# Kernel tuning notes

Hardware: AMD Instinct MI355X
Metric: run time of the kernel (lower is better)

The kernel has to match this reference:

```python
import jax, jax.numpy as jnp
import numpy as np


def _conv1d(x, w, b, pad):
    # x: (BN, Cin, L), w: (Cout, Cin, K) torch OIH layout
    y = jax.lax.conv_general_dilated(x, w, window_strides=(1,), padding=[(pad, pad)],
                                     dimension_numbers=('NCH', 'OIH', 'NCH'))
    return y + b[None, :, None]


def _mask_conv(m, k):
    # all-ones kernel conv then >=1 threshold (matches constant-init mask convs, no_grad)
    w = jnp.ones((1, 1, k), m.dtype)
    y = jax.lax.conv_general_dilated(m, w, window_strides=(1,), padding=[((k - 1) // 2, (k - 1) // 2)],
                                     dimension_numbers=('NCH', 'OIH', 'NCH'))
    return (y >= 1.0).astype(m.dtype)


def _branch(x, m, w1, b1, w2, b2, k):
    pad = (k - 1) // 2
    o = jax.nn.relu(_conv1d(x, w1, b1, pad))
    m = jax.lax.stop_gradient(_mask_conv(m, k))
    o = o * m
    o = jax.nn.relu(_conv1d(o, w2, b2, pad))
    m = jax.lax.stop_gradient(_mask_conv(m, k))
    return o * m


def _forward(all_xanes, all_xanes_mask, all_elem_info, all_elem_mask,
             w_b1c1, b_b1c1, w_b1c2, b_b1c2,
             w_b2c1, b_b2c1, w_b2c2, b_b2c2,
             w_b3c1, b_b3c1, w_b3c2, b_b3c2,
             w_xfc, b_xfc,
             w_float, b_float, atom_emb, type_emb,
             w_fuse, b_fuse,
             in_w, in_b, out_w, out_b,
             w_fc1, b_fc1, w_fc2, b_fc2):
    B, N, L = all_xanes.shape
    E, H = 64, 4
    dh = E // H
    # ---- MultiScaleXANESExtractor ----
    x = all_xanes.reshape(B * N, 1, L)
    m3 = jnp.broadcast_to(all_xanes_mask.reshape(B * N, 1, 1).astype(jnp.float32), (B * N, 1, L))
    o1 = _branch(x, m3, w_b1c1, b_b1c1, w_b1c2, b_b1c2, 3)
    o2 = _branch(x, m3, w_b2c1, b_b2c1, w_b2c2, b_b2c2, 5)
    o3 = _branch(x, m3, w_b3c1, b_b3c1, w_b3c2, b_b3c2, 7)
    cat = jnp.concatenate([o1, o2, o3], axis=1)  # (BN, 384, L)
    pooled = cat.reshape(B * N, 384, 10, L // 10).mean(-1).reshape(B * N, -1)  # AdaptiveAvgPool1d(10)
    xfeat = (pooled @ w_xfc.T + b_xfc).reshape(B, N, -1)  # (B, N, 32)
    valid = (m3.sum(axis=(1, 2)) > 0).astype(jnp.float32).reshape(B, N, 1)
    xfeat = xfeat * valid
    # ---- ElementsFeatureProcessor (vectorized gathers) ----
    maskf = all_elem_mask.astype(jnp.float32)
    masked = all_elem_info * maskf[..., None]
    ff = jax.nn.relu(masked[..., :5] @ w_float.T + b_float)  # (B, N, 16)
    an = masked[..., 5].astype(jnp.int32)
    et = masked[..., 6].astype(jnp.int32)
    valid_e = (maskf >= 0.5)
    inrange = (an >= 1) & (an <= 94)
    take = (valid_e & inrange).astype(jnp.float32)[..., None]
    ez = atom_emb[jnp.clip(an, 0, 94)] * take            # (B, N, 8)
    ety = type_emb[jnp.clip(et, 0, 5)] * take            # (B, N, 4)
    ff = ff * valid_e.astype(jnp.float32)[..., None]
    efeat = jnp.concatenate([ff, ez, ety], axis=-1) * maskf[..., None]  # (B, N, 28)
    # ---- FuseElementAndXANES ----
    fused = jnp.concatenate([xfeat, efeat], axis=-1) @ w_fuse.T + b_fuse
    fused = fused * maskf[..., None]  # (B, N, 64)
    # ---- AttentionAggregator (nn.MultiheadAttention, batch_first) ----
    qkv = fused @ in_w.T + in_b
    q, k, v = jnp.split(qkv, 3, axis=-1)
    q = q.reshape(B, N, H, dh)
    k = k.reshape(B, N, H, dh)
    v = v.reshape(B, N, H, dh)
    scores = jnp.einsum('bqhd,bkhd->bhqk', q, k) / jnp.sqrt(jnp.float32(dh))
    keymask = (maskf >= 0.5)
    scores = jnp.where(keymask[:, None, None, :], scores, jnp.float32(-1e30))
    attn = jax.nn.softmax(scores, axis=-1)
    ao = jnp.einsum('bhqk,bkhd->bqhd', attn, v).reshape(B, N, E)
    ao = ao @ out_w.T + out_b
    ao = ao * maskf[..., None]
    pooled2 = ao.sum(axis=1) / (maskf.sum(axis=1, keepdims=True) + 1e-8)
    h = jax.nn.relu(pooled2 @ w_fc1.T + b_fc1)
    return h @ w_fc2.T + b_fc2  # (B, num_classes)


def setup_inputs():
    key = jax.random.key(0)
    ks = jax.random.split(key, 40)
    B, N, L = 32, 16, 200
    all_xanes = jax.random.normal(ks[0], (B, N, L), jnp.float32)
    all_xanes_mask = jax.random.randint(ks[1], (B, N), 0, 2).astype(jnp.float32)
    ef = jax.random.normal(ks[2], (B, N, 7), jnp.float32)
    an = jax.random.randint(ks[3], (B, N), 1, 95).astype(jnp.float32)
    et = jax.random.randint(ks[4], (B, N), 0, 6).astype(jnp.float32)
    all_elem_info = ef.at[..., 5].set(an).at[..., 6].set(et)
    all_elem_mask = jax.random.randint(ks[5], (B, N), 0, 2).astype(jnp.float32)
    all_elem_mask = all_elem_mask.at[:, 0].set(1.0)  # avoid fully-padded rows (NaN softmax)

    def p(k, shape):
        return jax.random.normal(k, shape, jnp.float32) * 0.05

    inp = dict(all_xanes=all_xanes, all_xanes_mask=all_xanes_mask,
               all_elem_info=all_elem_info, all_elem_mask=all_elem_mask,
               w_b1c1=p(ks[6], (64, 1, 3)), b_b1c1=p(ks[7], (64,)),
               w_b1c2=p(ks[8], (128, 64, 3)), b_b1c2=p(ks[9], (128,)),
               w_b2c1=p(ks[10], (64, 1, 5)), b_b2c1=p(ks[11], (64,)),
               w_b2c2=p(ks[12], (128, 64, 5)), b_b2c2=p(ks[13], (128,)),
               w_b3c1=p(ks[14], (64, 1, 7)), b_b3c1=p(ks[15], (64,)),
               w_b3c2=p(ks[16], (128, 64, 7)), b_b3c2=p(ks[17], (128,)),
               w_xfc=p(ks[18], (32, 3840)), b_xfc=p(ks[19], (32,)),
               w_float=p(ks[20], (16, 5)), b_float=p(ks[21], (16,)),
               atom_emb=p(ks[22], (95, 8)), type_emb=p(ks[23], (6, 4)),
               w_fuse=p(ks[24], (64, 60)), b_fuse=p(ks[25], (64,)),
               in_w=p(ks[26], (192, 64)), in_b=p(ks[27], (192,)),
               out_w=p(ks[28], (64, 64)), out_b=p(ks[29], (64,)),
               w_fc1=p(ks[30], (64, 64)), b_fc1=p(ks[31], (64,)),
               w_fc2=p(ks[32], (1, 64)), b_fc2=p(ks[33], (1,)))
    return inp


def reference(all_xanes, all_xanes_mask, all_elem_info, all_elem_mask,
              w_b1c1, b_b1c1, w_b1c2, b_b1c2,
              w_b2c1, b_b2c1, w_b2c2, b_b2c2,
              w_b3c1, b_b3c1, w_b3c2, b_b3c2,
              w_xfc, b_xfc, w_float, b_float, atom_emb, type_emb,
              w_fuse, b_fuse, in_w, in_b, out_w, out_b,
              w_fc1, b_fc1, w_fc2, b_fc2):
    return _forward(all_xanes, all_xanes_mask, all_elem_info, all_elem_mask,
                    w_b1c1, b_b1c1, w_b1c2, b_b1c2,
                    w_b2c1, b_b2c1, w_b2c2, b_b2c2,
                    w_b3c1, b_b3c1, w_b3c2, b_b3c2,
                    w_xfc, b_xfc, w_float, b_float, atom_emb, type_emb,
                    w_fuse, b_fuse, in_w, in_b, out_w, out_b,
                    w_fc1, b_fc1, w_fc2, b_fc2)
```

## Files before the change

### kernel.cpp

```cpp
#include <hip/hip_runtime.h>
#include <math.h>

typedef float f32x4 __attribute__((ext_vector_type(4)));
typedef short short8 __attribute__((ext_vector_type(8)));

__device__ __forceinline__ short bf16r(float f) {
    union { float f; unsigned u; } x; x.f = f;
    unsigned u = x.u + 0x7fffu + ((x.u >> 16) & 1u);
    return (short)(u >> 16);
}

template<int K>
__device__ __forceinline__ void pack_branch(const float* __restrict__ w2,
                                            short* __restrict__ wpack, int u) {
    int lane = u & 63;
    int kb   = (u >> 6) & 1;
    int rem  = u >> 7;
    int j = rem % K, c = rem / K;
    int co  = c * 16 + (lane & 15);
    int cib = kb * 32 + 8 * ((lane >> 4) & 3);
    short8 v;
    #pragma unroll
    for (int i = 0; i < 8; ++i)
        v[i] = bf16r(w2[(co * 64 + (cib + i)) * K + j]);
    *reinterpret_cast<short8*>(wpack + (size_t)u * 8) = v;
}

__global__ __launch_bounds__(256) void pack_kernel(
    const float* __restrict__ w23, const float* __restrict__ w25,
    const float* __restrict__ w27,
    short* __restrict__ wp3, short* __restrict__ wp5, short* __restrict__ wp7)
{
    int tid = blockIdx.x * 256 + threadIdx.x;
    const int n3 = 8 * 3 * 2 * 64;
    const int n5 = 8 * 5 * 2 * 64;
    const int n7 = 8 * 7 * 2 * 64;
    if (tid < n3)                pack_branch<3>(w23, wp3, tid);
    else if (tid < n3 + n5)      pack_branch<5>(w25, wp5, tid - n3);
    else if (tid < n3 + n5 + n7) pack_branch<7>(w27, wp7, tid - n3 - n5);
}

template<int K, int LT0, int NLT>
__device__ __forceinline__ void mfma_pass2(
    const short* __restrict__ t1s,
    const short8* __restrict__ wpB0, const short8* __restrict__ wpB1,
    int lane, f32x4* accA, f32x4* accB)
{
    constexpr int PAD = (K - 1) / 2;
    const int lane15 = lane & 15;
    const int g8 = 8 * ((lane >> 4) & 3);
    short8 bA = wpB0[0], bB = wpB1[0];
    #pragma unroll 1
    for (int m = 0; m < 2 * K - 1; ++m) {
        const short8 nA = wpB0[(m + 1) * 64];
        const short8 nB = wpB1[(m + 1) * 64];
        const int j = m >> 1, kb = m & 1;
        const int r = LT0 * 16 + lane15 + 3 + j - PAD;
        const int col = (kb * 32 + g8) ^ ((r & 7) << 3);
        const short* ab = &t1s[r * 64 + col];
        #pragma unroll
        for (int lt = 0; lt < NLT; ++lt) {
            const short8 af = *reinterpret_cast<const short8*>(ab + lt * 1024);
            accA[lt] = __builtin_amdgcn_mfma_f32_16x16x32_bf16(af, bA, accA[lt], 0, 0, 0);
            accB[lt] = __builtin_amdgcn_mfma_f32_16x16x32_bf16(af, bB, accB[lt], 0, 0, 0);
        }
        bA = nA; bB = nB;
    }
    {
        const int m = 2 * K - 1;
        const int j = m >> 1, kb = m & 1;
        const int r = LT0 * 16 + lane15 + 3 + j - PAD;
        const int col = (kb * 32 + g8) ^ ((r & 7) << 3);
        const short* ab = &t1s[r * 64 + col];
        #pragma unroll
        for (int lt = 0; lt < NLT; ++lt) {
            const short8 af = *reinterpret_cast<const short8*>(ab + lt * 1024);
            accA[lt] = __builtin_amdgcn_mfma_f32_16x16x32_bf16(af, bA, accA[lt], 0, 0, 0);
            accB[lt] = __builtin_amdgcn_mfma_f32_16x16x32_bf16(af, bB, accB[lt], 0, 0, 0);
        }
    }
}

template<int GV, int LT0, int NLT>
__device__ __forceinline__ void pool_accum(const f32x4* acc, float bb, float* pb) {
    #pragma unroll
    for (int lt = 0; lt < NLT; ++lt) {
        #pragma unroll
        for (int r4 = 0; r4 < 4; ++r4) {
            const int l = (LT0 + lt) * 16 + 4 * GV + r4;
            if (l < 200)
                pb[l / 20] += fmaxf(acc[lt][r4] + bb, 0.0f);
        }
    }
}

template<int K, int LT0, int NLT>
__device__ __forceinline__ void do_pass2(
    const short* __restrict__ t1s,
    const short8* __restrict__ wpB0, const short8* __restrict__ wpB1,
    int lane, float bb0, float bb1, float* pb0, float* pb1)
{
    const int g = (lane >> 4) & 3;
    f32x4 accA[NLT], accB[NLT];
    #pragma unroll
    for (int i = 0; i < NLT; ++i) {
        f32x4 z = {0.f, 0.f, 0.f, 0.f};
        accA[i] = z; accB[i] = z;
    }
    mfma_pass2<K, LT0, NLT>(t1s, wpB0, wpB1, lane, accA, accB);
    if      (g == 0) { pool_accum<0, LT0, NLT>(accA, bb0, pb0); pool_accum<0, LT0, NLT>(accB, bb1, pb1); }
    else if (g == 1) { pool_accum<1, LT0, NLT>(accA, bb0, pb0); pool_accum<1, LT0, NLT>(accB, bb1, pb1); }
    else if (g == 2) { pool_accum<2, LT0, NLT>(accA, bb0, pb0); pool_accum<2, LT0, NLT>(accB, bb1, pb1); }
    else             { pool_accum<3, LT0, NLT>(accA, bb0, pb0); pool_accum<3, LT0, NLT>(accB, bb1, pb1); }
}

template<int K>
__device__ __forceinline__ void branch_body(
    const int bn, const int t,
    const float* __restrict__ x,
    const float* __restrict__ w1, const float* __restrict__ b1,
    const float* __restrict__ b2, const short* __restrict__ wpack,
    const float* __restrict__ w_xfc_br, float* __restrict__ xfeatP_br,
    float* xs, short* t1s, float* pooled_s, float* b2s)
{
    constexpr int PAD = (K - 1) / 2;
    const int lane = t & 63;
    const int w    = t >> 6;
    const int lane15 = lane & 15;

    if (t < 208) xs[t] = 0.0f;
    for (int idx = t; idx < 32 * 64; idx += 256) {
        int rr = idx >> 6;
        int row = (rr < 3) ? rr : (200 + rr);
        t1s[row * 64 + (idx & 63)] = 0;
    }
    if (t < 128) b2s[t] = b2[t];
    __syncthreads();

    if (t < 200) xs[3 + t] = x[bn * 200 + t];
    __syncthreads();

    {
        float w1_0 = w1[lane * K + 0], w1_1 = w1[lane * K + 1], w1_2 = w1[lane * K + 2];
        float w1_3 = 0.f, w1_4 = 0.f, w1_5 = 0.f, w1_6 = 0.f;
        if (K > 3) { w1_3 = w1[lane * K + 3]; w1_4 = w1[lane * K + 4]; }
        if (K > 5) { w1_5 = w1[lane * K + 5]; w1_6 = w1[lane * K + 6]; }
        const float b1r = b1[lane];
        #pragma unroll 1
        for (int ch = 0; ch < 2; ++ch) {
            const int lb = 50 * w + 25 * ch;
            float xr[31];
            #pragma unroll
            for (int i = 0; i < 31; ++i) xr[i] = xs[lb + i];
            #pragma unroll
            for (int ll = 0; ll < 25; ++ll) {
                float a = b1r;
                a = fmaf(w1_0, xr[ll + 3 - PAD + 0], a);
                a = fmaf(w1_1, xr[ll + 3 - PAD + 1], a);
                a = fmaf(w1_2, xr[ll + 3 - PAD + 2], a);
                if (K > 3) {
                    a = fmaf(w1_3, xr[ll + 3 - PAD + 3], a);
                    a = fmaf(w1_4, xr[ll + 3 - PAD + 4], a);
                }
                if (K > 5) {
                    a = fmaf(w1_5, xr[ll + 3 - PAD + 5], a);
                    a = fmaf(w1_6, xr[ll + 3 - PAD + 6], a);
                }
                const int row = lb + ll + 3;
                t1s[row * 64 + (lane ^ ((row & 7) << 3))] = bf16r(fmaxf(a, 0.0f));
            }
        }
    }
    __syncthreads();

    const int c0 = 2 * w, c1 = 2 * w + 1;
    const int coA = c0 * 16 + lane15, coB = c1 * 16 + lane15;
    const float bb0 = b2s[coA], bb1 = b2s[coB];
    const short8* wpB0 = reinterpret_cast<const short8*>(wpack)
                         + (size_t)(c0 * 2 * K) * 64 + lane;
    const short8* wpB1 = reinterpret_cast<const short8*>(wpack)
                         + (size_t)(c1 * 2 * K) * 64 + lane;

    float pb0[10], pb1[10];
    #pragma unroll
    for (int b = 0; b < 10; ++b) { pb0[b] = 0.0f; pb1[b] = 0.0f; }

    do_pass2<K, 0, 7>(t1s, wpB0, wpB1, lane, bb0, bb1, pb0, pb1);
    do_pass2<K, 7, 6>(t1s, wpB0, wpB1, lane, bb0, bb1, pb0, pb1);

    #pragma unroll
    for (int b = 0; b < 10; ++b) {
        pb0[b] += __shfl_xor(pb0[b], 16);
        pb0[b] += __shfl_xor(pb0[b], 32);
        pb1[b] += __shfl_xor(pb1[b], 16);
        pb1[b] += __shfl_xor(pb1[b], 32);
    }
    if (lane < 16) {
        #pragma unroll
        for (int b = 0; b < 10; ++b) {
            pooled_s[coA * 10 + b] = pb0[b];
            pooled_s[coB * 10 + b] = pb1[b];
        }
    }
    __syncthreads();

    {
        const int o = t >> 3, part = t & 7;
        const f32x4* wr4 = reinterpret_cast<const f32x4*>(w_xfc_br + o * 3840);
        const f32x4* pp4 = reinterpret_cast<const f32x4*>(pooled_s);
        float s0 = 0.0f, s1 = 0.0f;
        #pragma unroll
        for (int i = 0; i < 40; ++i) {
            const f32x4 wv = wr4[part + 8 * i];
            const f32x4 pv = pp4[part + 8 * i];
            float s = wv[0] * pv[0];
            s = fmaf(wv[1], pv[1], s);
            s = fmaf(wv[2], pv[2], s);
            s = fmaf(wv[3], pv[3], s);
            if (i & 1) s1 += s; else s0 += s;
        }
        float a = s0 + s1;
        a += __shfl_xor(a, 1);
        a += __shfl_xor(a, 2);
        a += __shfl_xor(a, 4);
        if (part == 0) xfeatP_br[bn * 32 + o] = a * 0.05f;
    }
}

__global__ __launch_bounds__(256, 4) void branch_fused(
    const float* __restrict__ x, const float* __restrict__ xmask,
    const float* __restrict__ w1_3, const float* __restrict__ b1_3,
    const float* __restrict__ b2_3, const short* __restrict__ wp3,
    const float* __restrict__ w1_5, const float* __restrict__ b1_5,
    const float* __restrict__ b2_5, const short* __restrict__ wp5,
    const float* __restrict__ w1_7, const float* __restrict__ b1_7,
    const float* __restrict__ b2_7, const short* __restrict__ wp7,
    const float* __restrict__ w_xfc, float* __restrict__ xfeatP)
{
    __shared__ float xs[208];
    __shared__ short t1s[232 * 64];
    __shared__ __align__(16) float pooled_s[1280];
    __shared__ float b2s[128];

    const int bx = blockIdx.x;
    const int br = bx % 3;
    const int bn = bx / 3;
    const int t  = threadIdx.x;

    if (xmask[bn] == 0.0f) return;

    if (br == 0)
        branch_body<3>(bn, t, x, w1_3, b1_3, b2_3, wp3,
                       w_xfc,        xfeatP,             xs, t1s, pooled_s, b2s);
    else if (br == 1)
        branch_body<5>(bn, t, x, w1_5, b1_5, b2_5, wp5,
                       w_xfc + 1280, xfeatP + 512 * 32,  xs, t1s, pooled_s, b2s);
    else
        branch_body<7>(bn, t, x, w1_7, b1_7, b2_7, wp7,
                       w_xfc + 2560, xfeatP + 1024 * 32, xs, t1s, pooled_s, b2s);
}

__global__ __launch_bounds__(256, 1) void tail_kernel(
    const float* __restrict__ xfeatP,
    const float* __restrict__ b_xfc,
    const float* __restrict__ xmaskp,
    const float* __restrict__ elem_info,
    const float* __restrict__ emaskp,
    const float* __restrict__ w_float, const float* __restrict__ b_float,
    const float* __restrict__ atom_emb, const float* __restrict__ type_emb,
    const float* __restrict__ w_fuse,  const float* __restrict__ b_fuse,
    const float* __restrict__ in_w,    const float* __restrict__ in_b,
    const float* __restrict__ out_w,   const float* __restrict__ out_b,
    const float* __restrict__ w_fc1,   const float* __restrict__ b_fc1,
    const float* __restrict__ w_fc2,   const float* __restrict__ b_fc2,
    float* __restrict__ out)
{
    const int b = blockIdx.x;
    const int t = threadIdx.x;

    __shared__ __align__(16) float fu[16][60];
    __shared__ __align__(16) float fused[16][64];
    __shared__ __align__(16) float qkvs[16][196];
    __shared__ __align__(16) float sc[4][16][16];
    __shared__ __align__(16) float ao[16][64];
    __shared__ __align__(16) float aoo[16][64];
    __shared__ float p2s[64];
    __shared__ float hs[64];
    __shared__ float em[16];

    if (t < 16) em[t] = emaskp[b * 16 + t];

    for (int d = t; d < 512; d += 256) {
        int n = d >> 5, o = d & 31;
        const int bn = b * 16 + n;
        float a = xfeatP[bn * 32 + o]
                + xfeatP[(512 + bn) * 32 + o]
                + xfeatP[(1024 + bn) * 32 + o];
        fu[n][o] = (a + b_xfc[o]) * xmaskp[bn];
    }
    {
        int n = t >> 4, slot = t & 15;
        float m  = emaskp[b * 16 + n];
        float vE = (m >= 0.5f) ? 1.0f : 0.0f;
        const float* ei = elem_info + (b * 16 + n) * 7;
        float a = b_float[slot];
        #pragma unroll
        for (int i = 0; i < 5; ++i)
            a = fmaf(ei[i] * m, w_float[slot * 5 + i], a);
        fu[n][32 + slot] = fmaxf(a, 0.0f) * vE * m;

        int an = (int)(ei[5] * m);
        int et = (int)(ei[6] * m);
        float take = (vE != 0.0f && an >= 1 && an <= 94) ? 1.0f : 0.0f;
        int anc = an < 0 ? 0 : (an > 94 ? 94 : an);
        int etc = et < 0 ? 0 : (et > 5 ? 5 : et);
        if (slot < 8)
            fu[n][48 + slot] = atom_emb[anc * 8 + slot] * take * m;
        else if (slot < 12)
            fu[n][56 + (slot - 8)] = type_emb[etc * 4 + (slot - 8)] * take * m;
    }
    __syncthreads();

    for (int d = t; d < 1024; d += 256) {
        int n = d >> 6, o = d & 63;
        const f32x4* wr4 = reinterpret_cast<const f32x4*>(w_fuse + o * 60);
        const f32x4* fr4 = reinterpret_cast<const f32x4*>(&fu[n][0]);
        float a0 = b_fuse[o], a1 = 0.0f;
        #pragma unroll
        for (int i = 0; i < 15; ++i) {
            const f32x4 wv = wr4[i];
            const f32x4 fv = fr4[i];
            float s = wv[0] * fv[0];
            s = fmaf(wv[1], fv[1], s);
            s = fmaf(wv[2], fv[2], s);
            s = fmaf(wv[3], fv[3], s);
            if (i & 1) a1 += s; else a0 += s;
        }
        fused[n][o] = (a0 + a1) * em[n];
    }
    __syncthreads();

    for (int d = t; d < 3072; d += 256) {
        int n = d / 192, rr = d - n * 192;
        const f32x4* wr4 = reinterpret_cast<const f32x4*>(in_w + rr * 64);
        const f32x4* fr4 = reinterpret_cast<const f32x4*>(&fused[n][0]);
        float a0 = in_b[rr], a1 = 0.0f;
        #pragma unroll
        for (int i = 0; i < 16; ++i) {
            const f32x4 wv = wr4[i];
            const f32x4 fv = fr4[i];
            float s = wv[0] * fv[0];
            s = fmaf(wv[1], fv[1], s);
            s = fmaf(wv[2], fv[2], s);
            s = fmaf(wv[3], fv[3], s);
            if (i & 1) a1 += s; else a0 += s;
        }
        qkvs[n][rr] = a0 + a1;
    }
    __syncthreads();

    for (int d = t; d < 1024; d += 256) {
        int h = d >> 8, i = (d >> 4) & 15, j = d & 15;
        const f32x4* qi = reinterpret_cast<const f32x4*>(&qkvs[i][h * 16]);
        const f32x4* kj = reinterpret_cast<const f32x4*>(&qkvs[j][64 + h * 16]);
        float a = 0.0f;
        #pragma unroll
        for (int q4 = 0; q4 < 4; ++q4) {
            const f32x4 qv = qi[q4];
            const f32x4 kv = kj[q4];
            a = fmaf(qv[0], kv[0], a);
            a = fmaf(qv[1], kv[1], a);
            a = fmaf(qv[2], kv[2], a);
            a = fmaf(qv[3], kv[3], a);
        }
        a *= 0.25f;
        if (em[j] < 0.5f) a = -1e30f;
        sc[h][i][j] = a;
    }
    __syncthreads();

    if (t < 64) {
        int h = t >> 4, i = t & 15;
        float mx = -3.4e38f;
        #pragma unroll
        for (int j = 0; j < 16; ++j) mx = fmaxf(mx, sc[h][i][j]);
        float e[16];
        float s = 0.0f;
        #pragma unroll
        for (int j = 0; j < 16; ++j) { e[j] = expf(sc[h][i][j] - mx); s += e[j]; }
        float inv = 1.0f / s;
        #pragma unroll
        for (int j = 0; j < 16; ++j) sc[h][i][j] = e[j] * inv;
    }
    __syncthreads();

    for (int d = t; d < 1024; d += 256) {
        int n = d >> 6, e = d & 63, h = e >> 4;
        float a = 0.0f;
        #pragma unroll
        for (int j = 0; j < 16; ++j)
            a = fmaf(sc[h][n][j], qkvs[j][128 + e], a);
        ao[n][e] = a;
    }
    __syncthreads();

    for (int d = t; d < 1024; d += 256) {
        int n = d >> 6, o = d & 63;
        const f32x4* wr4 = reinterpret_cast<const f32x4*>(out_w + o * 64);
        const f32x4* ar4 = reinterpret_cast<const f32x4*>(&ao[n][0]);
        float a0 = out_b[o], a1 = 0.0f;
        #pragma unroll
        for (int i = 0; i < 16; ++i) {
            const f32x4 wv = wr4[i];
            const f32x4 av = ar4[i];
            float s = wv[0] * av[0];
            s = fmaf(wv[1], av[1], s);
            s = fmaf(wv[2], av[2], s);
            s = fmaf(wv[3], av[3], s);
            if (i & 1) a1 += s; else a0 += s;
        }
        aoo[n][o] = (a0 + a1) * em[n];
    }
    __syncthreads();

    if (t < 64) {
        float s = 0.0f, ms = 0.0f;
        #pragma unroll
        for (int n = 0; n < 16; ++n) { s += aoo[n][t]; ms += em[n]; }
        p2s[t] = s / (ms + 1e-8f);
    }
    __syncthreads();

    if (t < 64) {
        const f32x4* wr4 = reinterpret_cast<const f32x4*>(w_fc1 + t * 64);
        const f32x4* pr4 = reinterpret_cast<const f32x4*>(p2s);
        float a0 = b_fc1[t], a1 = 0.0f;
        #pragma unroll
        for (int i = 0; i < 16; ++i) {
            const f32x4 wv = wr4[i];
            const f32x4 pv = pr4[i];
            float s = wv[0] * pv[0];
            s = fmaf(wv[1], pv[1], s);
            s = fmaf(wv[2], pv[2], s);
            s = fmaf(wv[3], pv[3], s);
            if (i & 1) a1 += s; else a0 += s;
        }
        hs[t] = fmaxf(a0 + a1, 0.0f);
    }
    __syncthreads();

    if (t < 64) {
        float v = hs[t] * w_fc2[t];
        #pragma unroll
        for (int d2 = 32; d2 >= 1; d2 >>= 1) v += __shfl_xor(v, d2);
        if (t == 0) out[b] = v + b_fc2[0];
    }
}

extern "C" void kernel_launch(void* const* d_in, const int* in_sizes, int n_in,
                              void* d_out, int out_size, void* d_ws, size_t ws_size,
                              hipStream_t stream)
{
    (void)in_sizes; (void)n_in; (void)out_size; (void)ws_size;
    const float* x     = (const float*)d_in[0];
    const float* xmask = (const float*)d_in[1];
    const float* einfo = (const float*)d_in[2];
    const float* emask = (const float*)d_in[3];

    float* xfeatP = (float*)d_ws;
    short* wp3 = (short*)(xfeatP + 3 * 512 * 32);
    short* wp5 = wp3 + 24576;
    short* wp7 = wp5 + 40960;

    pack_kernel<<<60, 256, 0, stream>>>(
        (const float*)d_in[6], (const float*)d_in[10], (const float*)d_in[14],
        wp3, wp5, wp7);

    branch_fused<<<1536, 256, 0, stream>>>(x, xmask,
        (const float*)d_in[4],  (const float*)d_in[5],  (const float*)d_in[7],  wp3,
        (const float*)d_in[8],  (const float*)d_in[9],  (const float*)d_in[11], wp5,
        (const float*)d_in[12], (const float*)d_in[13], (const float*)d_in[15], wp7,
        (const float*)d_in[16], xfeatP);

    tail_kernel<<<32, 256, 0, stream>>>(xfeatP,
        (const float*)d_in[17], xmask, einfo, emask,
        (const float*)d_in[18], (const float*)d_in[19],
        (const float*)d_in[20], (const float*)d_in[21],
        (const float*)d_in[22], (const float*)d_in[23],
        (const float*)d_in[24], (const float*)d_in[25],
        (const float*)d_in[26], (const float*)d_in[27],
        (const float*)d_in[28], (const float*)d_in[29],
        (const float*)d_in[30], (const float*)d_in[31],
        (float*)d_out);
}
```

Before: 70.19 us.

## Fuse branch and tail kernels into one launch with per-batch completion counters

Merges the branch convolution kernel and the tail attention kernel into a single persistent-style launch. The first 32 blocks spin-wait on per-batch atomic counters until all 48 branch blocks for their batch have finished, then run the tail. The goal is to drop one kernel launch and let tail work for early batches overlap with the remaining branch work. In exchange it adds a memset, atomic polling and threadfences, and relies on the spinning tail blocks not starving the branch blocks of CU slots. The shared memory union is also sized to the larger of the two stages, which may affect occupancy.

```diff
diff --git a/kernel.cpp b/kernel.cpp
--- a/kernel.cpp
+++ b/kernel.cpp
@@ -227,44 +227,10 @@
     }
 }
 
-__global__ __launch_bounds__(256, 4) void branch_fused(
-    const float* __restrict__ x, const float* __restrict__ xmask,
-    const float* __restrict__ w1_3, const float* __restrict__ b1_3,
-    const float* __restrict__ b2_3, const short* __restrict__ wp3,
-    const float* __restrict__ w1_5, const float* __restrict__ b1_5,
-    const float* __restrict__ b2_5, const short* __restrict__ wp5,
-    const float* __restrict__ w1_7, const float* __restrict__ b1_7,
-    const float* __restrict__ b2_7, const short* __restrict__ wp7,
-    const float* __restrict__ w_xfc, float* __restrict__ xfeatP)
-{
-    __shared__ float xs[208];
-    __shared__ short t1s[232 * 64];
-    __shared__ __align__(16) float pooled_s[1280];
-    __shared__ float b2s[128];
-
-    const int bx = blockIdx.x;
-    const int br = bx % 3;
-    const int bn = bx / 3;
-    const int t  = threadIdx.x;
-
-    if (xmask[bn] == 0.0f) return;
-
-    if (br == 0)
-        branch_body<3>(bn, t, x, w1_3, b1_3, b2_3, wp3,
-                       w_xfc,        xfeatP,             xs, t1s, pooled_s, b2s);
-    else if (br == 1)
-        branch_body<5>(bn, t, x, w1_5, b1_5, b2_5, wp5,
-                       w_xfc + 1280, xfeatP + 512 * 32,  xs, t1s, pooled_s, b2s);
-    else
-        branch_body<7>(bn, t, x, w1_7, b1_7, b2_7, wp7,
-                       w_xfc + 2560, xfeatP + 1024 * 32, xs, t1s, pooled_s, b2s);
-}
-
-__global__ __launch_bounds__(256, 1) void tail_kernel(
-    const float* __restrict__ xfeatP,
-    const float* __restrict__ b_xfc,
-    const float* __restrict__ xmaskp,
-    const float* __restrict__ elem_info,
+__device__ void tail_body(
+    const int b, const int t, char* smem,
+    const float* __restrict__ xfeatP, const float* __restrict__ b_xfc,
+    const float* __restrict__ xmaskp, const float* __restrict__ elem_info,
     const float* __restrict__ emaskp,
     const float* __restrict__ w_float, const float* __restrict__ b_float,
     const float* __restrict__ atom_emb, const float* __restrict__ type_emb,
@@ -275,18 +241,19 @@
     const float* __restrict__ w_fc2,   const float* __restrict__ b_fc2,
     float* __restrict__ out)
 {
-    const int b = blockIdx.x;
-    const int t = threadIdx.x;
-
-    __shared__ __align__(16) float fu[16][60];
-    __shared__ __align__(16) float fused[16][64];
-    __shared__ __align__(16) float qkvs[16][196];
-    __shared__ __align__(16) float sc[4][16][16];
-    __shared__ __align__(16) float ao[16][64];
-    __shared__ __align__(16) float aoo[16][64];
-    __shared__ float p2s[64];
-    __shared__ float hs[64];
-    __shared__ float em[16];
+    typedef float fu_t[60];
+    typedef float f64_t[64];
+    typedef float q_t[196];
+    typedef float sc_t[16][16];
+    fu_t*  fu    = (fu_t*) (smem + 0);
+    f64_t* fused = (f64_t*)(smem + 3840);
+    q_t*   qkvs  = (q_t*)  (smem + 7936);
+    sc_t*  sc    = (sc_t*) (smem + 20480);
+    f64_t* ao    = (f64_t*)(smem + 24576);
+    f64_t* aoo   = (f64_t*)(smem + 28672);
+    float* p2s   = (float*)(smem + 32768);
+    float* hs    = (float*)(smem + 33024);
+    float* em    = (float*)(smem + 33280);
 
     if (t < 16) em[t] = emaskp[b * 16 + t];
 
@@ -457,6 +424,70 @@
     }
 }
 
+__global__ __launch_bounds__(256, 4) void mega(
+    const float* __restrict__ x, const float* __restrict__ xmask,
+    const float* __restrict__ w1_3, const float* __restrict__ b1_3,
+    const float* __restrict__ b2_3, const short* __restrict__ wp3,
+    const float* __restrict__ w1_5, const float* __restrict__ b1_5,
+    const float* __restrict__ b2_5, const short* __restrict__ wp5,
+    const float* __restrict__ w1_7, const float* __restrict__ b1_7,
+    const float* __restrict__ b2_7, const short* __restrict__ wp7,
+    const float* __restrict__ w_xfc, float* __restrict__ xfeatP,
+    unsigned* __restrict__ cnts,
+    const float* __restrict__ b_xfc,
+    const float* __restrict__ elem_info, const float* __restrict__ emaskp,
+    const float* __restrict__ w_float, const float* __restrict__ b_float,
+    const float* __restrict__ atom_emb, const float* __restrict__ type_emb,
+    const float* __restrict__ w_fuse,  const float* __restrict__ b_fuse,
+    const float* __restrict__ in_w,    const float* __restrict__ in_b,
+    const float* __restrict__ out_w,   const float* __restrict__ out_b,
+    const float* __restrict__ w_fc1,   const float* __restrict__ b_fc1,
+    const float* __restrict__ w_fc2,   const float* __restrict__ b_fc2,
+    float* __restrict__ out)
+{
+    __shared__ __align__(16) char smem[36608];
+    const int bx = blockIdx.x;
+    const int t  = threadIdx.x;
+
+    if (bx < 32) {
+        const int b = bx;
+        if (t == 0) {
+            while (atomicAdd(&cnts[b], 0u) < 48u)
+                __builtin_amdgcn_s_sleep(8);
+        }
+        __syncthreads();
+        __threadfence();
+        tail_body(b, t, smem, xfeatP, b_xfc, xmask, elem_info, emaskp,
+                  w_float, b_float, atom_emb, type_emb, w_fuse, b_fuse,
+                  in_w, in_b, out_w, out_b, w_fc1, b_fc1, w_fc2, b_fc2, out);
+        return;
+    }
+
+    const int pbx = bx - 32;
+    const int br  = pbx % 3;
+    const int bn  = pbx / 3;
+
+    float* xs       = (float*)(smem + 0);
+    short* t1s      = (short*)(smem + 832);
+    float* pooled_s = (float*)(smem + 30528);
+    float* b2s      = (float*)(smem + 35648);
+
+    if (xmask[bn] != 0.0f) {
+        if (br == 0)
+            branch_body<3>(bn, t, x, w1_3, b1_3, b2_3, wp3,
+                           w_xfc,        xfeatP,             xs, t1s, pooled_s, b2s);
+        else if (br == 1)
+            branch_body<5>(bn, t, x, w1_5, b1_5, b2_5, wp5,
+                           w_xfc + 1280, xfeatP + 512 * 32,  xs, t1s, pooled_s, b2s);
+        else
+            branch_body<7>(bn, t, x, w1_7, b1_7, b2_7, wp7,
+                           w_xfc + 2560, xfeatP + 1024 * 32, xs, t1s, pooled_s, b2s);
+        __threadfence();
+    }
+    __syncthreads();
+    if (t == 0) atomicAdd(&cnts[bn >> 4], 1u);
+}
+
 extern "C" void kernel_launch(void* const* d_in, const int* in_sizes, int n_in,
                               void* d_out, int out_size, void* d_ws, size_t ws_size,
                               hipStream_t stream)
@@ -467,23 +498,24 @@
     const float* einfo = (const float*)d_in[2];
     const float* emask = (const float*)d_in[3];
 
-    float* xfeatP = (float*)d_ws;
-    short* wp3 = (short*)(xfeatP + 3 * 512 * 32);
-    short* wp5 = wp3 + 24576;
-    short* wp7 = wp5 + 40960;
+    float*    xfeatP = (float*)d_ws;
+    short*    wp3  = (short*)((char*)d_ws + 196608);
+    short*    wp5  = wp3 + 24576;
+    short*    wp7  = wp5 + 40960;
+    unsigned* cnts = (unsigned*)((char*)d_ws + 442368);
+
+    hipMemsetAsync(cnts, 0, 32 * sizeof(unsigned), stream);
 
     pack_kernel<<<60, 256, 0, stream>>>(
         (const float*)d_in[6], (const float*)d_in[10], (const float*)d_in[14],
         wp3, wp5, wp7);
 
-    branch_fused<<<1536, 256, 0, stream>>>(x, xmask,
+    mega<<<1568, 256, 0, stream>>>(x, xmask,
         (const float*)d_in[4],  (const float*)d_in[5],  (const float*)d_in[7],  wp3,
         (const float*)d_in[8],  (const float*)d_in[9],  (const float*)d_in[11], wp5,
         (const float*)d_in[12], (const float*)d_in[13], (const float*)d_in[15], wp7,
-        (const float*)d_in[16], xfeatP);
-
-    tail_kernel<<<32, 256, 0, stream>>>(xfeatP,
-        (const float*)d_in[17], xmask, einfo, emask,
+        (const float*)d_in[16], xfeatP, cnts,
+        (const float*)d_in[17], einfo, emask,
         (const float*)d_in[18], (const float*)d_in[19],
         (const float*)d_in[20], (const float*)d_in[21],
         (const float*)d_in[22], (const float*)d_in[23],
```

Result: slower. 167.9 us (+139.2%).

## Split each conv branch block into two sequence halves for more parallelism

Applied to the files above, without the earlier changes.

Each (sample, branch) block is split into two blocks, each covering half of the 200-length sequence. Each half computes its own conv1 rows plus a halo, then runs MFMA conv2 over 6 or 7 row tiles and writes a partial pooled projection into one of six workspace slices, which the tail kernel sums. This doubles the grid and roughly halves the LDS per block, aiming at better occupancy and load balance. The cost is redundant halo conv1 work, duplicated per-block setup, and extra workspace traffic.

```diff
diff --git a/kernel.cpp b/kernel.cpp
--- a/kernel.cpp
+++ b/kernel.cpp
@@ -40,7 +40,7 @@
     else if (tid < n3 + n5 + n7) pack_branch<7>(w27, wp7, tid - n3 - n5);
 }
 
-template<int K, int LT0, int NLT>
+template<int K, int NLT>
 __device__ __forceinline__ void mfma_pass2(
     const short* __restrict__ t1s,
     const short8* __restrict__ wpB0, const short8* __restrict__ wpB1,
@@ -55,7 +55,7 @@
         const short8 nA = wpB0[(m + 1) * 64];
         const short8 nB = wpB1[(m + 1) * 64];
         const int j = m >> 1, kb = m & 1;
-        const int r = LT0 * 16 + lane15 + 3 + j - PAD;
+        const int r = lane15 + 3 + j - PAD;
         const int col = (kb * 32 + g8) ^ ((r & 7) << 3);
         const short* ab = &t1s[r * 64 + col];
         #pragma unroll
@@ -69,7 +69,7 @@
     {
         const int m = 2 * K - 1;
         const int j = m >> 1, kb = m & 1;
-        const int r = LT0 * 16 + lane15 + 3 + j - PAD;
+        const int r = lane15 + 3 + j - PAD;
         const int col = (kb * 32 + g8) ^ ((r & 7) << 3);
         const short* ab = &t1s[r * 64 + col];
         #pragma unroll
@@ -107,31 +107,37 @@
         f32x4 z = {0.f, 0.f, 0.f, 0.f};
         accA[i] = z; accB[i] = z;
     }
-    mfma_pass2<K, LT0, NLT>(t1s, wpB0, wpB1, lane, accA, accB);
+    mfma_pass2<K, NLT>(t1s, wpB0, wpB1, lane, accA, accB);
     if      (g == 0) { pool_accum<0, LT0, NLT>(accA, bb0, pb0); pool_accum<0, LT0, NLT>(accB, bb1, pb1); }
     else if (g == 1) { pool_accum<1, LT0, NLT>(accA, bb0, pb0); pool_accum<1, LT0, NLT>(accB, bb1, pb1); }
     else if (g == 2) { pool_accum<2, LT0, NLT>(accA, bb0, pb0); pool_accum<2, LT0, NLT>(accB, bb1, pb1); }
     else             { pool_accum<3, LT0, NLT>(accA, bb0, pb0); pool_accum<3, LT0, NLT>(accB, bb1, pb1); }
 }
 
-template<int K>
+template<int K, int HALF>
 __device__ __forceinline__ void branch_body(
     const int bn, const int t,
     const float* __restrict__ x,
     const float* __restrict__ w1, const float* __restrict__ b1,
     const float* __restrict__ b2, const short* __restrict__ wpack,
-    const float* __restrict__ w_xfc_br, float* __restrict__ xfeatP_br,
+    const float* __restrict__ w_xfc_br, float* __restrict__ xfeatP_sl,
     float* xs, short* t1s, float* pooled_s, float* b2s)
 {
-    constexpr int PAD = (K - 1) / 2;
+    constexpr int PAD  = (K - 1) / 2;
+    constexpr int ROFF = HALF ? 93 : -3;
+    constexpr int C0   = HALF ? 93 : 0;
+    constexpr int C1   = HALF ? 200 : 99;
+    constexpr int LT0  = HALF ? 6 : 0;
+    constexpr int NT   = HALF ? 7 : 6;
+
     const int lane = t & 63;
     const int w    = t >> 6;
     const int lane15 = lane & 15;
 
     if (t < 208) xs[t] = 0.0f;
-    for (int idx = t; idx < 32 * 64; idx += 256) {
+    for (int idx = t; idx < 16 * 64; idx += 256) {
         int rr = idx >> 6;
-        int row = (rr < 3) ? rr : (200 + rr);
+        int row = (rr < 3) ? rr : (104 + rr);
         t1s[row * 64 + (idx & 63)] = 0;
     }
     if (t < 128) b2s[t] = b2[t];
@@ -146,29 +152,16 @@
         if (K > 3) { w1_3 = w1[lane * K + 3]; w1_4 = w1[lane * K + 4]; }
         if (K > 5) { w1_5 = w1[lane * K + 5]; w1_6 = w1[lane * K + 6]; }
         const float b1r = b1[lane];
-        #pragma unroll 1
-        for (int ch = 0; ch < 2; ++ch) {
-            const int lb = 50 * w + 25 * ch;
-            float xr[31];
-            #pragma unroll
-            for (int i = 0; i < 31; ++i) xr[i] = xs[lb + i];
-            #pragma unroll
-            for (int ll = 0; ll < 25; ++ll) {
-                float a = b1r;
-                a = fmaf(w1_0, xr[ll + 3 - PAD + 0], a);
-                a = fmaf(w1_1, xr[ll + 3 - PAD + 1], a);
-                a = fmaf(w1_2, xr[ll + 3 - PAD + 2], a);
-                if (K > 3) {
-                    a = fmaf(w1_3, xr[ll + 3 - PAD + 3], a);
-                    a = fmaf(w1_4, xr[ll + 3 - PAD + 4], a);
-                }
-                if (K > 5) {
-                    a = fmaf(w1_5, xr[ll + 3 - PAD + 5], a);
-                    a = fmaf(w1_6, xr[ll + 3 - PAD + 6], a);
-                }
-                const int row = lb + ll + 3;
-                t1s[row * 64 + (lane ^ ((row & 7) << 3))] = bf16r(fmaxf(a, 0.0f));
-            }
+        for (int l = C0 + w; l < C1; l += 4) {
+            const float* xp = &xs[3 + l - PAD];
+            float a = b1r;
+            a = fmaf(w1_0, xp[0], a);
+            a = fmaf(w1_1, xp[1], a);
+            a = fmaf(w1_2, xp[2], a);
+            if (K > 3) { a = fmaf(w1_3, xp[3], a); a = fmaf(w1_4, xp[4], a); }
+            if (K > 5) { a = fmaf(w1_5, xp[5], a); a = fmaf(w1_6, xp[6], a); }
+            const int row = l - ROFF;
+            t1s[row * 64 + (lane ^ ((row & 7) << 3))] = bf16r(fmaxf(a, 0.0f));
         }
     }
     __syncthreads();
@@ -185,8 +178,7 @@
     #pragma unroll
     for (int b = 0; b < 10; ++b) { pb0[b] = 0.0f; pb1[b] = 0.0f; }
 
-    do_pass2<K, 0, 7>(t1s, wpB0, wpB1, lane, bb0, bb1, pb0, pb1);
-    do_pass2<K, 7, 6>(t1s, wpB0, wpB1, lane, bb0, bb1, pb0, pb1);
+    do_pass2<K, LT0, NT>(t1s, wpB0, wpB1, lane, bb0, bb1, pb0, pb1);
 
     #pragma unroll
     for (int b = 0; b < 10; ++b) {
@@ -223,7 +215,7 @@
         a += __shfl_xor(a, 1);
         a += __shfl_xor(a, 2);
         a += __shfl_xor(a, 4);
-        if (part == 0) xfeatP_br[bn * 32 + o] = a * 0.05f;
+        if (part == 0) xfeatP_sl[bn * 32 + o] = a * 0.05f;
     }
 }
 
@@ -238,26 +230,30 @@
     const float* __restrict__ w_xfc, float* __restrict__ xfeatP)
 {
     __shared__ float xs[208];
-    __shared__ short t1s[232 * 64];
+    __shared__ short t1s[120 * 64];
     __shared__ __align__(16) float pooled_s[1280];
     __shared__ float b2s[128];
 
     const int bx = blockIdx.x;
-    const int br = bx % 3;
-    const int bn = bx / 3;
+    const int s  = bx % 6;
+    const int bn = bx / 6;
+    const int br = s >> 1;
+    const int hf = s & 1;
     const int t  = threadIdx.x;
 
     if (xmask[bn] == 0.0f) return;
 
-    if (br == 0)
-        branch_body<3>(bn, t, x, w1_3, b1_3, b2_3, wp3,
-                       w_xfc,        xfeatP,             xs, t1s, pooled_s, b2s);
-    else if (br == 1)
-        branch_body<5>(bn, t, x, w1_5, b1_5, b2_5, wp5,
-                       w_xfc + 1280, xfeatP + 512 * 32,  xs, t1s, pooled_s, b2s);
-    else
-        branch_body<7>(bn, t, x, w1_7, b1_7, b2_7, wp7,
-                       w_xfc + 2560, xfeatP + 1024 * 32, xs, t1s, pooled_s, b2s);
+    float* sl = xfeatP + (size_t)s * 512 * 32;
+    if (br == 0) {
+        if (hf == 0) branch_body<3,0>(bn, t, x, w1_3, b1_3, b2_3, wp3, w_xfc,        sl, xs, t1s, pooled_s, b2s);
+        else         branch_body<3,1>(bn, t, x, w1_3, b1_3, b2_3, wp3, w_xfc,        sl, xs, t1s, pooled_s, b2s);
+    } else if (br == 1) {
+        if (hf == 0) branch_body<5,0>(bn, t, x, w1_5, b1_5, b2_5, wp5, w_xfc + 1280, sl, xs, t1s, pooled_s, b2s);
+        else         branch_body<5,1>(bn, t, x, w1_5, b1_5, b2_5, wp5, w_xfc + 1280, sl, xs, t1s, pooled_s, b2s);
+    } else {
+        if (hf == 0) branch_body<7,0>(bn, t, x, w1_7, b1_7, b2_7, wp7, w_xfc + 2560, sl, xs, t1s, pooled_s, b2s);
+        else         branch_body<7,1>(bn, t, x, w1_7, b1_7, b2_7, wp7, w_xfc + 2560, sl, xs, t1s, pooled_s, b2s);
+    }
 }
 
 __global__ __launch_bounds__(256, 1) void tail_kernel(
@@ -293,9 +289,10 @@
     for (int d = t; d < 512; d += 256) {
         int n = d >> 5, o = d & 31;
         const int bn = b * 16 + n;
-        float a = xfeatP[bn * 32 + o]
-                + xfeatP[(512 + bn) * 32 + o]
-                + xfeatP[(1024 + bn) * 32 + o];
+        float a = 0.0f;
+        #pragma unroll
+        for (int s = 0; s < 6; ++s)
+            a += xfeatP[(s * 512 + bn) * 32 + o];
         fu[n][o] = (a + b_xfc[o]) * xmaskp[bn];
     }
     {
@@ -468,7 +465,7 @@
     const float* emask = (const float*)d_in[3];
 
     float* xfeatP = (float*)d_ws;
-    short* wp3 = (short*)(xfeatP + 3 * 512 * 32);
+    short* wp3 = (short*)(xfeatP + 6 * 512 * 32);
     short* wp5 = wp3 + 24576;
     short* wp7 = wp5 + 40960;
 
@@ -476,7 +473,7 @@
         (const float*)d_in[6], (const float*)d_in[10], (const float*)d_in[14],
         wp3, wp5, wp7);
 
-    branch_fused<<<1536, 256, 0, stream>>>(x, xmask,
+    branch_fused<<<3072, 256, 0, stream>>>(x, xmask,
         (const float*)d_in[4],  (const float*)d_in[5],  (const float*)d_in[7],  wp3,
         (const float*)d_in[8],  (const float*)d_in[9],  (const float*)d_in[11], wp5,
         (const float*)d_in[12], (const float*)d_in[13], (const float*)d_in[15], wp7,
```

Result: no change. 71.31 us (+1.6%).
